# Kernel optimization log

Hardware: AMD Instinct MI355X
Metric: run time of the kernel (lower is better)

Reference implementation:

```python
import jax, jax.numpy as jnp
import numpy as np

TOP_K = 2

def setup_inputs() -> dict:
    key = jax.random.key(0)
    ks = jax.random.split(key, 6)
    B, T, D, H, E = 2, 1024, 1024, 4096, 32
    s = 0.02  # weight init scale
    return {
        "x": jax.random.normal(ks[0], (B, T, D), jnp.float32),
        "gate_w": jax.random.normal(ks[1], (E, D), jnp.float32) * s,
        "bias": jnp.zeros((E,), jnp.float32),
        "shared_w1": jax.random.normal(ks[2], (D, H // 2), jnp.float32) * s,
        "shared_w2": jax.random.normal(ks[3], (H // 2, D), jnp.float32) * s,
        "expert_w1": jax.random.normal(ks[4], (E, D, H), jnp.float32) * s,
        "expert_w2": jax.random.normal(ks[5], (E, H, D), jnp.float32) * s,
    }

def reference(x, gate_w, bias, shared_w1, shared_w2, expert_w1, expert_w2):
    B, T, D = x.shape
    xf = x.reshape(-1, D)                      # [N, D], N = B*T
    N = xf.shape[0]
    E = gate_w.shape[0]

    # shared expert (SwiGLU-less SiLU MLP, hidden_dim // 2)
    shared = jax.nn.silu(xf @ shared_w1) @ shared_w2

    # routing: sigmoid gate + correction bias, top-k, normalize
    scores = jax.nn.sigmoid(xf @ gate_w.T) + bias          # [N, E]
    topk_w, topk_idx = jax.lax.top_k(scores, TOP_K)        # [N, K]
    topk_w = topk_w / (topk_w.sum(-1, keepdims=True) + 1e-20)

    # dense combine weights: w_full[n, e] = topk weight if expert e chosen else 0
    w_full = jnp.zeros((N, E), xf.dtype).at[
        jnp.arange(N)[:, None], topk_idx
    ].set(topk_w)                                          # [N, E]

    # scan over experts: each expert runs its MLP, combine-weighted accumulate
    def step(acc, ws):
        w1, w2, we = ws                                    # [D,H], [H,D], [N]
        return acc + we[:, None] * (jax.nn.silu(xf @ w1) @ w2), None

    sparse, _ = jax.lax.scan(step, jnp.zeros_like(xf),
                             (expert_w1, expert_w2, w_full.T))
    return (shared + sparse).reshape(B, T, D)
```

## Files before the change

### kernel.cpp

```cpp
#include <hip/hip_runtime.h>
#include <hip/hip_bf16.h>

typedef __attribute__((ext_vector_type(8))) short short8;
typedef __attribute__((ext_vector_type(4))) float floatx4;

#define BM 256
#define BN 128
#define BK 32
#define CAP 256
#define NEXP 32
#define NTOK 2048
#define DDIM 1024
#define HDIM 4096
#define HSH 2048

__device__ __forceinline__ void g2lds16(const void* g, void* l) {
  __builtin_amdgcn_global_load_lds((const __attribute__((address_space(1))) void*)g,
                                   (__attribute__((address_space(3))) void*)l, 16, 0, 0);
}

__device__ __forceinline__ short f2bf(float f) {
  union { __hip_bfloat16 h; unsigned short u; } c;
  c.h = __float2bfloat16(f);
  return (short)c.u;
}

__global__ __launch_bounds__(256)
void gate_kernel(const float* __restrict__ x, const float* __restrict__ gate_w,
                 const float* __restrict__ bias,
                 __hip_bfloat16* __restrict__ xbf, __hip_bfloat16* __restrict__ Xg,
                 int* __restrict__ counts, int* __restrict__ assign_token,
                 float* __restrict__ assign_w) {
  const int wv = threadIdx.x >> 6, lane = threadIdx.x & 63;
  const int n = blockIdx.x * 4 + wv;
  const float4* xr = reinterpret_cast<const float4*>(x + (size_t)n * DDIM);
  float4 xv0 = xr[lane * 4 + 0], xv1 = xr[lane * 4 + 1];
  float4 xv2 = xr[lane * 4 + 2], xv3 = xr[lane * 4 + 3];

  float best = -1e30f, second = -1e30f; int bi = 0, si = 0;
  for (int e = 0; e < NEXP; e++) {
    const float4* gw = reinterpret_cast<const float4*>(gate_w + (size_t)e * DDIM);
    float4 g0 = gw[lane * 4 + 0], g1 = gw[lane * 4 + 1];
    float4 g2 = gw[lane * 4 + 2], g3 = gw[lane * 4 + 3];
    float s = g0.x*xv0.x + g0.y*xv0.y + g0.z*xv0.z + g0.w*xv0.w
            + g1.x*xv1.x + g1.y*xv1.y + g1.z*xv1.z + g1.w*xv1.w
            + g2.x*xv2.x + g2.y*xv2.y + g2.z*xv2.z + g2.w*xv2.w
            + g3.x*xv3.x + g3.y*xv3.y + g3.z*xv3.z + g3.w*xv3.w;
    #pragma unroll
    for (int off = 32; off > 0; off >>= 1) s += __shfl_xor(s, off);
    s = 1.f / (1.f + expf(-s)) + bias[e];
    if (s > best)        { second = best; si = bi; best = s; bi = e; }
    else if (s > second) { second = s; si = e; }
  }
  float denom = best + second + 1e-20f;
  float w0 = best / denom, w1 = second / denom;

  short8 p0, p1;
  p0[0]=f2bf(xv0.x); p0[1]=f2bf(xv0.y); p0[2]=f2bf(xv0.z); p0[3]=f2bf(xv0.w);
  p0[4]=f2bf(xv1.x); p0[5]=f2bf(xv1.y); p0[6]=f2bf(xv1.z); p0[7]=f2bf(xv1.w);
  p1[0]=f2bf(xv2.x); p1[1]=f2bf(xv2.y); p1[2]=f2bf(xv2.z); p1[3]=f2bf(xv2.w);
  p1[4]=f2bf(xv3.x); p1[5]=f2bf(xv3.y); p1[6]=f2bf(xv3.z); p1[7]=f2bf(xv3.w);

  short8* xo = (short8*)(xbf + (size_t)n * DDIM);
  xo[lane * 2] = p0; xo[lane * 2 + 1] = p1;

  int slot0 = -1, slot1 = -1;
  if (lane == 0) {
    int p = atomicAdd(&counts[bi], 1);
    if (p < CAP) slot0 = bi * CAP + p;
    p = atomicAdd(&counts[si], 1);
    if (p < CAP) slot1 = si * CAP + p;
  }
  slot0 = __shfl(slot0, 0); slot1 = __shfl(slot1, 0);
  if (slot0 >= 0) {
    if (lane == 0) { assign_token[slot0] = n; assign_w[slot0] = w0; }
    short8* o = (short8*)(Xg + (size_t)slot0 * DDIM);
    o[lane * 2] = p0; o[lane * 2 + 1] = p1;
  }
  if (slot1 >= 0) {
    if (lane == 0) { assign_token[slot1] = n; assign_w[slot1] = w1; }
    short8* o = (short8*)(Xg + (size_t)slot1 * DDIM);
    o[lane * 2] = p0; o[lane * 2 + 1] = p1;
  }
}

template<int EPI>
__global__ __launch_bounds__(256, 2)
void gemm_kernel(const __hip_bfloat16* __restrict__ A, size_t a_blk_stride,
                 const float* __restrict__ B, size_t b_blk_stride,
                 int K, int Ksplit, int ldB, int ldC,
                 float* __restrict__ outF, __hip_bfloat16* __restrict__ outH,
                 const int* __restrict__ assign_token,
                 const float* __restrict__ assign_w) {
  __shared__ __align__(16) __hip_bfloat16 sA[BM * BK];
  __shared__ __align__(16) unsigned char sB[BN * 80];

  const int tid = threadIdx.x;
  const int wv = tid >> 6, lane = tid & 63;
  const int bx = blockIdx.x, by = blockIdx.y, bz = blockIdx.z;
  const int rl = lane & 15, qd = lane >> 4;

  const __hip_bfloat16* Ab = A + (size_t)by * a_blk_stride;
  const float* Bb = B + (size_t)by * b_blk_stride + (size_t)bx * BN;

  floatx4 acc[4][8];
  #pragma unroll
  for (int m = 0; m < 4; m++)
    #pragma unroll
    for (int ns = 0; ns < 8; ns++) acc[m][ns] = (floatx4){0.f, 0.f, 0.f, 0.f};

  const int bn0 = (tid & 31) * 4;
  const int bkq = tid >> 5;
  const int k_begin = bz * Ksplit, k_end = k_begin + Ksplit;

  for (int k0 = k_begin; k0 < k_end; k0 += BK) {
    #pragma unroll
    for (int i = 0; i < 4; i++) {
      int c = (i * 4 + wv) * 64 + lane;
      int row = c >> 2, q = c & 3;
      const __hip_bfloat16* gp = Ab + (size_t)row * K + k0 + q * 8;
      g2lds16((const void*)gp, (void*)(sA + (size_t)(i * 4 + wv) * 512));
    }
    if (tid < 128) {
      const float* bp = Bb + (size_t)(k0 + bkq * 8) * ldB + bn0;
      float4 rr[8];
      #pragma unroll
      for (int j = 0; j < 8; j++) rr[j] = *(const float4*)(bp + (size_t)j * ldB);
      #pragma unroll
      for (int jj = 0; jj < 4; jj++) {
        int n = bn0 + jj;
        short8 v;
        #pragma unroll
        for (int i = 0; i < 8; i++) v[i] = f2bf(((const float*)&rr[i])[jj]);
        int qp = bkq ^ (((n >> 2) + (n >> 4)) & 3);
        *(short8*)(sB + (size_t)n * 80 + qp * 16) = v;
      }
    }
    __syncthreads();

    short8 af[4];
    #pragma unroll
    for (int m = 0; m < 4; m++) {
      int row = wv * 64 + m * 16 + rl;
      af[m] = *(const short8*)((const unsigned char*)sA + (size_t)row * 64 + qd * 16);
    }
    short8 bfr[8];
    #pragma unroll
    for (int ns = 0; ns < 8; ns++) {
      int n = ns * 16 + rl;
      int qp = qd ^ (((n >> 2) + (n >> 4)) & 3);
      bfr[ns] = *(const short8*)(sB + (size_t)n * 80 + qp * 16);
    }
    #pragma unroll
    for (int m = 0; m < 4; m++)
      #pragma unroll
      for (int ns = 0; ns < 8; ns++)
        acc[m][ns] = __builtin_amdgcn_mfma_f32_16x16x32_bf16(af[m], bfr[ns], acc[m][ns], 0, 0, 0);
    __syncthreads();
  }

  const int colbase = bx * BN;
  #pragma unroll
  for (int m = 0; m < 4; m++) {
    #pragma unroll
    for (int r = 0; r < 4; r++) {
      int row = wv * 64 + m * 16 + qd * 4 + r;
      if (EPI == 0) {
        #pragma unroll
        for (int ns = 0; ns < 8; ns++) {
          float v = acc[m][ns][r];
          float sv = v / (1.f + __expf(-v));
          outH[((size_t)by * BM + row) * ldC + colbase + ns * 16 + rl] = __float2bfloat16(sv);
        }
      } else if (EPI == 1) {
        int slot = by * BM + row;
        int tok = assign_token[slot];
        if (tok >= 0) {
          float wgt = assign_w[slot];
          #pragma unroll
          for (int ns = 0; ns < 8; ns++)
            atomicAdd(outF + (size_t)tok * ldC + colbase + ns * 16 + rl, wgt * acc[m][ns][r]);
        }
      } else {
        #pragma unroll
        for (int ns = 0; ns < 8; ns++)
          atomicAdd(outF + ((size_t)by * BM + row) * ldC + colbase + ns * 16 + rl, acc[m][ns][r]);
      }
    }
  }
}

extern "C" void kernel_launch(void* const* d_in, const int* in_sizes, int n_in,
                              void* d_out, int out_size, void* d_ws, size_t ws_size,
                              hipStream_t stream) {
  const float* x         = (const float*)d_in[0];
  const float* gate_w    = (const float*)d_in[1];
  const float* bias      = (const float*)d_in[2];
  const float* shared_w1 = (const float*)d_in[3];
  const float* shared_w2 = (const float*)d_in[4];
  const float* expert_w1 = (const float*)d_in[5];
  const float* expert_w2 = (const float*)d_in[6];
  float* out = (float*)d_out;

  char* w = (char*)d_ws;
  int*   counts       = (int*)w;
  int*   assign_token = (int*)(w + 256);
  float* assign_w     = (float*)(w + 256 + 32768);
  size_t off = 256 + 32768 + 32768;
  __hip_bfloat16* xbf = (__hip_bfloat16*)(w + off); off += (size_t)NTOK * DDIM * 2;
  __hip_bfloat16* Xg  = (__hip_bfloat16*)(w + off); off += (size_t)NEXP * CAP * DDIM * 2;
  __hip_bfloat16* Hs  = (__hip_bfloat16*)(w + off); off += (size_t)NTOK * HSH * 2;
  __hip_bfloat16* H   = (__hip_bfloat16*)(w + off); off += (size_t)NEXP * CAP * HDIM * 2;

  hipMemsetAsync(counts, 0, 256, stream);
  hipMemsetAsync(assign_token, 0xFF, 32768, stream);
  hipMemsetAsync(d_out, 0, (size_t)out_size * 4, stream);

  gate_kernel<<<NTOK / 4, 256, 0, stream>>>(x, gate_w, bias, xbf, Xg,
                                            counts, assign_token, assign_w);

  gemm_kernel<0><<<dim3(HSH / BN, NTOK / BM, 1), 256, 0, stream>>>(
      xbf, (size_t)BM * DDIM, shared_w1, 0,
      DDIM, DDIM, HSH, HSH, nullptr, Hs, nullptr, nullptr);

  gemm_kernel<0><<<dim3(HDIM / BN, NEXP, 1), 256, 0, stream>>>(
      Xg, (size_t)CAP * DDIM, expert_w1, (size_t)DDIM * HDIM,
      DDIM, DDIM, HDIM, HDIM, nullptr, H, nullptr, nullptr);

  gemm_kernel<2><<<dim3(DDIM / BN, NTOK / BM, 4), 256, 0, stream>>>(
      Hs, (size_t)BM * HSH, shared_w2, 0,
      HSH, HSH / 4, DDIM, DDIM, out, nullptr, nullptr, nullptr);

  gemm_kernel<1><<<dim3(DDIM / BN, NEXP, 2), 256, 0, stream>>>(
      H, (size_t)CAP * HDIM, expert_w2, (size_t)HDIM * DDIM,
      HDIM, HDIM / 2, DDIM, DDIM, out, nullptr, assign_token, assign_w);
}
```

Baseline: 1.320 ms.

## Merge shared and expert GEMMs into grouped launches, skip empty rows, prefetch B

Replaces the four GEMM launches with two grouped kernels (fc1 covers shared and expert up-projections, fc2 covers both down-projections), so shared-expert and routed-expert tiles can run concurrently. Expert tiles read the per-expert token count and skip loading and computing row blocks beyond it, and return early for empty experts. The B-tile fp32 loads are now spread across all 256 threads and prefetched one K-step ahead into registers, overlapping global loads with MFMA work. The cost is some idle blocks that exit early, larger register pressure from the prefetch buffer, and divergent per-wave work when experts are partially filled.

```diff
diff --git a/kernel.cpp b/kernel.cpp
--- a/kernel.cpp
+++ b/kernel.cpp
@@ -2,6 +2,7 @@
 #include <hip/hip_bf16.h>
 
 typedef __attribute__((ext_vector_type(8))) short short8;
+typedef __attribute__((ext_vector_type(4))) short short4v;
 typedef __attribute__((ext_vector_type(4))) float floatx4;
 
 #define BM 256
@@ -84,24 +85,104 @@
   }
 }
 
-template<int EPI>
+__device__ __forceinline__ void gemm_core(
+    const __hip_bfloat16* __restrict__ Ab, int lda,
+    const float* __restrict__ Bb, int ldB,
+    int k_begin, int k_end, int liveM,
+    __hip_bfloat16* sA, unsigned char* sB, floatx4 (&acc)[4][8]) {
+  const int tid = threadIdx.x;
+  const int wv = tid >> 6, lane = tid & 63;
+  const int rl = lane & 15, qd = lane >> 4;
+  const int bn0 = (tid & 31) * 4;
+  const int bkr = (tid >> 5) * 4;
+  const int bq  = bkr >> 3;
+  const int bh  = (bkr >> 2) & 1;
+
+  float4 rr[4];
+  {
+    const float* bp = Bb + (size_t)(k_begin + bkr) * ldB + bn0;
+    #pragma unroll
+    for (int j = 0; j < 4; j++) rr[j] = *(const float4*)(bp + (size_t)j * ldB);
+  }
+
+  for (int k0 = k_begin; k0 < k_end; k0 += BK) {
+    #pragma unroll
+    for (int i = 0; i < 4; i++) {
+      int rowbase = (i * 4 + wv) * 16;
+      if (rowbase < liveM) {
+        int c = (i * 4 + wv) * 64 + lane;
+        int row = c >> 2, q = c & 3;
+        g2lds16((const void*)(Ab + (size_t)row * lda + k0 + q * 8),
+                (void*)(sA + (size_t)(i * 4 + wv) * 512));
+      }
+    }
+    #pragma unroll
+    for (int jj = 0; jj < 4; jj++) {
+      int n = bn0 + jj;
+      short4v v;
+      v[0] = f2bf(((const float*)&rr[0])[jj]);
+      v[1] = f2bf(((const float*)&rr[1])[jj]);
+      v[2] = f2bf(((const float*)&rr[2])[jj]);
+      v[3] = f2bf(((const float*)&rr[3])[jj]);
+      int qp = bq ^ (((n >> 2) + (n >> 4)) & 3);
+      *(short4v*)(sB + (size_t)n * 80 + qp * 16 + bh * 8) = v;
+    }
+    __syncthreads();
+    if (k0 + BK < k_end) {
+      const float* bp = Bb + (size_t)(k0 + BK + bkr) * ldB + bn0;
+      #pragma unroll
+      for (int j = 0; j < 4; j++) rr[j] = *(const float4*)(bp + (size_t)j * ldB);
+    }
+    if (wv * 64 < liveM) {
+      short8 bfr[8];
+      #pragma unroll
+      for (int ns = 0; ns < 8; ns++) {
+        int n = ns * 16 + rl;
+        int qp = qd ^ (((n >> 2) + (n >> 4)) & 3);
+        bfr[ns] = *(const short8*)(sB + (size_t)n * 80 + qp * 16);
+      }
+      #pragma unroll
+      for (int m = 0; m < 4; m++) {
+        if (wv * 64 + m * 16 < liveM) {
+          int row = wv * 64 + m * 16 + rl;
+          short8 af = *(const short8*)((const unsigned char*)sA + (size_t)row * 64 + qd * 16);
+          #pragma unroll
+          for (int ns = 0; ns < 8; ns++)
+            acc[m][ns] = __builtin_amdgcn_mfma_f32_16x16x32_bf16(af, bfr[ns], acc[m][ns], 0, 0, 0);
+        }
+      }
+    }
+    __syncthreads();
+  }
+}
+
 __global__ __launch_bounds__(256, 2)
-void gemm_kernel(const __hip_bfloat16* __restrict__ A, size_t a_blk_stride,
-                 const float* __restrict__ B, size_t b_blk_stride,
-                 int K, int Ksplit, int ldB, int ldC,
-                 float* __restrict__ outF, __hip_bfloat16* __restrict__ outH,
-                 const int* __restrict__ assign_token,
-                 const float* __restrict__ assign_w) {
+void fc1_kernel(const __hip_bfloat16* __restrict__ xbf, const __hip_bfloat16* __restrict__ Xg,
+                const float* __restrict__ sw1, const float* __restrict__ ew1,
+                __hip_bfloat16* __restrict__ Hs, __hip_bfloat16* __restrict__ H,
+                const int* __restrict__ counts) {
   __shared__ __align__(16) __hip_bfloat16 sA[BM * BK];
   __shared__ __align__(16) unsigned char sB[BN * 80];
-
-  const int tid = threadIdx.x;
-  const int wv = tid >> 6, lane = tid & 63;
-  const int bx = blockIdx.x, by = blockIdx.y, bz = blockIdx.z;
+  const int bx = blockIdx.x, by = blockIdx.y;
+  const int tid = threadIdx.x, wv = tid >> 6, lane = tid & 63;
   const int rl = lane & 15, qd = lane >> 4;
 
-  const __hip_bfloat16* Ab = A + (size_t)by * a_blk_stride;
-  const float* Bb = B + (size_t)by * b_blk_stride + (size_t)bx * BN;
+  const __hip_bfloat16* Ab; const float* Bb; __hip_bfloat16* Co;
+  int ldB, ldC, liveM;
+  if (by < NEXP) {
+    Ab = Xg + (size_t)by * CAP * DDIM;
+    Bb = ew1 + (size_t)by * DDIM * HDIM + (size_t)bx * BN; ldB = HDIM;
+    Co = H + (size_t)by * CAP * HDIM; ldC = HDIM;
+    liveM = min(counts[by], CAP);
+    if (liveM == 0) return;
+  } else {
+    if (bx >= HSH / BN) return;
+    int mb = by - NEXP;
+    Ab = xbf + (size_t)mb * BM * DDIM;
+    Bb = sw1 + (size_t)bx * BN; ldB = HSH;
+    Co = Hs + (size_t)mb * BM * HSH; ldC = HSH;
+    liveM = BM;
+  }
 
   floatx4 acc[4][8];
   #pragma unroll
@@ -109,82 +190,92 @@
     #pragma unroll
     for (int ns = 0; ns < 8; ns++) acc[m][ns] = (floatx4){0.f, 0.f, 0.f, 0.f};
 
-  const int bn0 = (tid & 31) * 4;
-  const int bkq = tid >> 5;
-  const int k_begin = bz * Ksplit, k_end = k_begin + Ksplit;
-
-  for (int k0 = k_begin; k0 < k_end; k0 += BK) {
-    #pragma unroll
-    for (int i = 0; i < 4; i++) {
-      int c = (i * 4 + wv) * 64 + lane;
-      int row = c >> 2, q = c & 3;
-      const __hip_bfloat16* gp = Ab + (size_t)row * K + k0 + q * 8;
-      g2lds16((const void*)gp, (void*)(sA + (size_t)(i * 4 + wv) * 512));
-    }
-    if (tid < 128) {
-      const float* bp = Bb + (size_t)(k0 + bkq * 8) * ldB + bn0;
-      float4 rr[8];
-      #pragma unroll
-      for (int j = 0; j < 8; j++) rr[j] = *(const float4*)(bp + (size_t)j * ldB);
-      #pragma unroll
-      for (int jj = 0; jj < 4; jj++) {
-        int n = bn0 + jj;
-        short8 v;
-        #pragma unroll
-        for (int i = 0; i < 8; i++) v[i] = f2bf(((const float*)&rr[i])[jj]);
-        int qp = bkq ^ (((n >> 2) + (n >> 4)) & 3);
-        *(short8*)(sB + (size_t)n * 80 + qp * 16) = v;
-      }
-    }
-    __syncthreads();
-
-    short8 af[4];
-    #pragma unroll
-    for (int m = 0; m < 4; m++) {
-      int row = wv * 64 + m * 16 + rl;
-      af[m] = *(const short8*)((const unsigned char*)sA + (size_t)row * 64 + qd * 16);
-    }
-    short8 bfr[8];
-    #pragma unroll
-    for (int ns = 0; ns < 8; ns++) {
-      int n = ns * 16 + rl;
-      int qp = qd ^ (((n >> 2) + (n >> 4)) & 3);
-      bfr[ns] = *(const short8*)(sB + (size_t)n * 80 + qp * 16);
-    }
-    #pragma unroll
-    for (int m = 0; m < 4; m++)
-      #pragma unroll
-      for (int ns = 0; ns < 8; ns++)
-        acc[m][ns] = __builtin_amdgcn_mfma_f32_16x16x32_bf16(af[m], bfr[ns], acc[m][ns], 0, 0, 0);
-    __syncthreads();
-  }
+  gemm_core(Ab, DDIM, Bb, ldB, 0, DDIM, liveM, sA, sB, acc);
 
   const int colbase = bx * BN;
   #pragma unroll
   for (int m = 0; m < 4; m++) {
-    #pragma unroll
-    for (int r = 0; r < 4; r++) {
-      int row = wv * 64 + m * 16 + qd * 4 + r;
-      if (EPI == 0) {
+    if (wv * 64 + m * 16 < liveM) {
+      #pragma unroll
+      for (int r = 0; r < 4; r++) {
+        int row = wv * 64 + m * 16 + qd * 4 + r;
         #pragma unroll
         for (int ns = 0; ns < 8; ns++) {
           float v = acc[m][ns][r];
           float sv = v / (1.f + __expf(-v));
-          outH[((size_t)by * BM + row) * ldC + colbase + ns * 16 + rl] = __float2bfloat16(sv);
+          Co[(size_t)row * ldC + colbase + ns * 16 + rl] = __float2bfloat16(sv);
         }
-      } else if (EPI == 1) {
-        int slot = by * BM + row;
-        int tok = assign_token[slot];
-        if (tok >= 0) {
-          float wgt = assign_w[slot];
-          #pragma unroll
-          for (int ns = 0; ns < 8; ns++)
-            atomicAdd(outF + (size_t)tok * ldC + colbase + ns * 16 + rl, wgt * acc[m][ns][r]);
+      }
+    }
+  }
+}
+
+__global__ __launch_bounds__(256, 2)
+void fc2_kernel(const __hip_bfloat16* __restrict__ H, const __hip_bfloat16* __restrict__ Hs,
+                const float* __restrict__ sw2, const float* __restrict__ ew2,
+                float* __restrict__ out, const int* __restrict__ counts,
+                const int* __restrict__ assign_token, const float* __restrict__ assign_w) {
+  __shared__ __align__(16) __hip_bfloat16 sA[BM * BK];
+  __shared__ __align__(16) unsigned char sB[BN * 80];
+  const int bx = blockIdx.x, by = blockIdx.y, bz = blockIdx.z;
+  const int tid = threadIdx.x, wv = tid >> 6, lane = tid & 63;
+  const int rl = lane & 15, qd = lane >> 4;
+  const bool isexp = (by < NEXP);
+
+  const __hip_bfloat16* Ab; const float* Bb;
+  int lda, kb, ke, liveM;
+  if (isexp) {
+    if (bz >= 2) return;
+    liveM = min(counts[by], CAP);
+    if (liveM == 0) return;
+    Ab = H + (size_t)by * CAP * HDIM; lda = HDIM;
+    Bb = ew2 + (size_t)by * HDIM * DDIM + (size_t)bx * BN;
+    kb = bz * (HDIM / 2); ke = kb + HDIM / 2;
+  } else {
+    int mb = by - NEXP;
+    Ab = Hs + (size_t)mb * BM * HSH; lda = HSH;
+    Bb = sw2 + (size_t)bx * BN;
+    kb = bz * (HSH / 4); ke = kb + HSH / 4;
+    liveM = BM;
+  }
+
+  floatx4 acc[4][8];
+  #pragma unroll
+  for (int m = 0; m < 4; m++)
+    #pragma unroll
+    for (int ns = 0; ns < 8; ns++) acc[m][ns] = (floatx4){0.f, 0.f, 0.f, 0.f};
+
+  gemm_core(Ab, lda, Bb, DDIM, kb, ke, liveM, sA, sB, acc);
+
+  const int colbase = bx * BN;
+  if (isexp) {
+    #pragma unroll
+    for (int m = 0; m < 4; m++) {
+      if (wv * 64 + m * 16 < liveM) {
+        #pragma unroll
+        for (int r = 0; r < 4; r++) {
+          int row = wv * 64 + m * 16 + qd * 4 + r;
+          int slot = by * CAP + row;
+          int tok = assign_token[slot];
+          if (tok >= 0) {
+            float wgt = assign_w[slot];
+            #pragma unroll
+            for (int ns = 0; ns < 8; ns++)
+              atomicAdd(out + (size_t)tok * DDIM + colbase + ns * 16 + rl, wgt * acc[m][ns][r]);
+          }
         }
-      } else {
+      }
+    }
+  } else {
+    int mb = by - NEXP;
+    #pragma unroll
+    for (int m = 0; m < 4; m++) {
+      #pragma unroll
+      for (int r = 0; r < 4; r++) {
+        int row = wv * 64 + m * 16 + qd * 4 + r;
         #pragma unroll
         for (int ns = 0; ns < 8; ns++)
-          atomicAdd(outF + ((size_t)by * BM + row) * ldC + colbase + ns * 16 + rl, acc[m][ns][r]);
+          atomicAdd(out + ((size_t)mb * BM + row) * DDIM + colbase + ns * 16 + rl, acc[m][ns][r]);
       }
     }
   }
@@ -219,19 +310,9 @@
   gate_kernel<<<NTOK / 4, 256, 0, stream>>>(x, gate_w, bias, xbf, Xg,
                                             counts, assign_token, assign_w);
 
-  gemm_kernel<0><<<dim3(HSH / BN, NTOK / BM, 1), 256, 0, stream>>>(
-      xbf, (size_t)BM * DDIM, shared_w1, 0,
-      DDIM, DDIM, HSH, HSH, nullptr, Hs, nullptr, nullptr);
-
-  gemm_kernel<0><<<dim3(HDIM / BN, NEXP, 1), 256, 0, stream>>>(
-      Xg, (size_t)CAP * DDIM, expert_w1, (size_t)DDIM * HDIM,
-      DDIM, DDIM, HDIM, HDIM, nullptr, H, nullptr, nullptr);
-
-  gemm_kernel<2><<<dim3(DDIM / BN, NTOK / BM, 4), 256, 0, stream>>>(
-      Hs, (size_t)BM * HSH, shared_w2, 0,
-      HSH, HSH / 4, DDIM, DDIM, out, nullptr, nullptr, nullptr);
-
-  gemm_kernel<1><<<dim3(DDIM / BN, NEXP, 2), 256, 0, stream>>>(
-      H, (size_t)CAP * HDIM, expert_w2, (size_t)HDIM * DDIM,
-      HDIM, HDIM / 2, DDIM, DDIM, out, nullptr, assign_token, assign_w);
-}
+  fc1_kernel<<<dim3(HDIM / BN, NEXP + NTOK / BM), 256, 0, stream>>>(
+      xbf, Xg, shared_w1, expert_w1, Hs, H, counts);
+
+  fc2_kernel<<<dim3(DDIM / BN, NEXP + NTOK / BM, 4), 256, 0, stream>>>(
+      H, Hs, shared_w2, expert_w2, out, counts, assign_token, assign_w);
+}
```

Result: faster. 1.175 ms (-11.0%).
